# Optimization experiments

Measured on AMD Instinct MI355X. Metric: run time of the kernel, lower is better.

Reference implementation:

```python
import jax, jax.numpy as jnp
import numpy as np

BATCH = 8192
IN_F = 1024
OUT_F = 1024
GRID = 5
K = 3            # spline order (degree)
SCALE = 1.0      # scale_spline


def setup_inputs() -> dict:
    key = jax.random.key(0)
    k1, k2, k3 = jax.random.split(key, 3)
    x = jax.random.normal(k1, (BATCH, IN_F), dtype=jnp.float32)
    # kaiming_uniform_(a=sqrt(5)) on (out,in) -> U(-1/sqrt(in), 1/sqrt(in))
    bound = 1.0 / np.sqrt(IN_F)
    base_weight = jax.random.uniform(k2, (OUT_F, IN_F), jnp.float32, -bound, bound)
    # normal(mean=0, std=0.1), shape (out, in, grid_size + spline_order)
    spline_weight = 0.1 * jax.random.normal(k3, (OUT_F, IN_F, GRID + K), dtype=jnp.float32)
    # extended knot vector: uniform grid on [-1,1] with spacing h, padded by K knots each side
    h = 2.0 / GRID
    knots = jnp.arange(-K, GRID + K + 1, dtype=jnp.float32) * h - 1.0  # (GRID+2K+1,)
    grid = jnp.tile(knots[None, :], (IN_F, 1))                          # (in, GRID+2K+1)
    return {"x": x, "base_weight": base_weight, "spline_weight": spline_weight, "grid": grid}


def _b_splines(x, grid, k):
    # x: (B, in), grid: (in, G+2k+1) -> basis: (B, in, G+k)
    xe = x[..., None]  # (B, in, 1)
    basis = ((xe >= grid[:, :-1]) & (xe < grid[:, 1:])).astype(x.dtype)  # degree-0, (B,in,G+2k)
    for p in range(1, k + 1):  # Cox-de Boor recursion, degree p
        left = (xe - grid[:, :-(p + 1)]) / (grid[:, p:-1] - grid[:, :-(p + 1)]) * basis[..., :-1]
        right = (grid[:, (p + 1):] - xe) / (grid[:, (p + 1):] - grid[:, 1:-p]) * basis[..., 1:]
        basis = left + right
    return basis


def reference(x, base_weight, spline_weight, grid):
    base = x @ base_weight.T                                   # (B, out)
    basis = _b_splines(x, grid, K)                             # (B, in, G+K)
    spline = jnp.einsum('bic,oic->bo', basis, spline_weight)   # (B, out)
    return base + SCALE * spline
```

## Files before the change

kernel.cpp:

```cpp
#include <hip/hip_runtime.h>


#define BATCH 8192
#define IN_F  1024
#define OUT_F 1024
#define NC    9
#define KAUG  (IN_F * NC)

typedef float  f32x4  __attribute__((ext_vector_type(4)));
typedef __bf16 bf16x8 __attribute__((ext_vector_type(8)));
typedef unsigned short u16;
typedef u16 u16x8 __attribute__((ext_vector_type(8)));

__device__ __forceinline__ u16 f2bf(float f) {
  unsigned int u = __builtin_bit_cast(unsigned int, f);
  u += 0x7FFFu + ((u >> 16) & 1u);
  return (u16)(u >> 16);
}

#define KT(j) ((float)((j) - 3) * 0.4f - 1.0f)

__device__ __forceinline__ void bspline8(float x, float bas[11]) {
#pragma unroll
  for (int j = 0; j < 11; ++j)
    bas[j] = (x >= KT(j) && x < KT(j + 1)) ? 1.0f : 0.0f;
#pragma unroll
  for (int p = 1; p <= 3; ++p) {
#pragma unroll
    for (int j = 0; j < 11 - p; ++j) {
      bas[j] = (x - KT(j)) * (1.0f / (KT(j + p) - KT(j))) * bas[j]
             + (KT(j + p + 1) - x) * (1.0f / (KT(j + p + 1) - KT(j + 1))) * bas[j + 1];
    }
  }
}

__global__ __launch_bounds__(256) void build_AW(const float* __restrict__ X,
                                                const float* __restrict__ BW,
                                                const float* __restrict__ SW,
                                                u16* __restrict__ Aa,
                                                u16* __restrict__ Wa) {
  const int idx = blockIdx.x * 256 + threadIdx.x;
  if (idx < BATCH * 128) {
    const int b  = idx >> 7;
    const int i0 = (idx & 127) << 3;
    const float4* xp = (const float4*)(X + (size_t)b * IN_F + i0);
    float4 xa = xp[0], xb = xp[1];
    float xs[8] = {xa.x, xa.y, xa.z, xa.w, xb.x, xb.y, xb.z, xb.w};
    u16x8 out[9];
#pragma unroll
    for (int e = 0; e < 8; ++e) {
      const float x = xs[e];
      out[0][e] = f2bf(x);
      float bas[11];
      bspline8(x, bas);
#pragma unroll
      for (int c = 0; c < 8; ++c) out[c + 1][e] = f2bf(bas[c]);
    }
    u16* row = Aa + (size_t)b * KAUG + i0;
#pragma unroll
    for (int c = 0; c < 9; ++c) *(u16x8*)(row + c * IN_F) = out[c];
  } else {
    const int wdx = idx - BATCH * 128;
    const int o  = wdx >> 7;
    const int i0 = (wdx & 127) << 3;
    u16x8 out[9];
    const float4* bp = (const float4*)(BW + (size_t)o * IN_F + i0);
    float4 b0 = bp[0], b1 = bp[1];
    float bs[8] = {b0.x, b0.y, b0.z, b0.w, b1.x, b1.y, b1.z, b1.w};
#pragma unroll
    for (int e = 0; e < 8; ++e) out[0][e] = f2bf(bs[e]);
    const float4* sp = (const float4*)(SW + ((size_t)o * IN_F + i0) * 8);
#pragma unroll
    for (int e = 0; e < 8; ++e) {
      float4 s0 = sp[e * 2], s1 = sp[e * 2 + 1];
      out[1][e] = f2bf(s0.x);
      out[2][e] = f2bf(s0.y);
      out[3][e] = f2bf(s0.z);
      out[4][e] = f2bf(s0.w);
      out[5][e] = f2bf(s1.x);
      out[6][e] = f2bf(s1.y);
      out[7][e] = f2bf(s1.z);
      out[8][e] = f2bf(s1.w);
    }
    u16* row = Wa + (size_t)o * KAUG + i0;
#pragma unroll
    for (int c = 0; c < 9; ++c) *(u16x8*)(row + c * IN_F) = out[c];
  }
}

#define BM 256
#define BN 128
#define BK 64
#define NT (KAUG / BK)

__device__ __forceinline__ void async16(const u16* g, u16* l) {
  __builtin_amdgcn_global_load_lds(
      (const __attribute__((address_space(1))) u16*)g,
      (__attribute__((address_space(3))) u16*)l,
      16, 0, 0);
}

__global__ __launch_bounds__(512) void gemm_bt(
    const u16* __restrict__ A,
    const u16* __restrict__ B,
    float* __restrict__ C) {
  constexpr int N = OUT_F, K = KAUG;
  __shared__ __align__(16) u16 sm[3][24576];

  const int tid = threadIdx.x;

  const int bid = blockIdx.x;
  const int wg  = (bid & 7) * 32 + (bid >> 3);
  const int bm  = wg >> 3;
  const int bn  = wg & 7;

  const int lane = tid & 63;
  const int wid  = tid >> 6;
  const int wm   = wid >> 1;
  const int wn   = wid & 1;
  const int fr   = lane & 15;
  const int hi   = lane >> 4;

  const int ak0 = ((hi      ^ (fr & 7)) << 3);
  const int ak1 = (((4 | hi) ^ (fr & 7)) << 3);
  int arow[4], brow[4];
#pragma unroll
  for (int m = 0; m < 4; ++m) arow[m] = (wm * 64 + m * 16 + fr) * 64;
#pragma unroll
  for (int n = 0; n < 4; ++n) brow[n] = 16384 + (wn * 64 + n * 16 + fr) * 64;

  const int trow = tid >> 3;
  const int gsrc = (tid & 7) ^ (trow & 7);
  const u16* Asrc = A + (size_t)(bm * BM + trow) * K + gsrc * 8;
  const u16* Bsrc = B + (size_t)(bn * BN + trow) * K + gsrc * 8;

#pragma unroll
  for (int tt = 0; tt < 2; ++tt) {
    u16* dA = &sm[tt][0] + tid * 8;
    u16* dB = &sm[tt][16384] + tid * 8;
    const size_t kg = (size_t)tt * BK;
    async16(Asrc + kg, dA);
    async16(Asrc + (size_t)64  * K + kg, dA + 4096);
    async16(Asrc + (size_t)128 * K + kg, dA + 8192);
    async16(Asrc + (size_t)192 * K + kg, dA + 12288);
    async16(Bsrc + kg, dB);
    async16(Bsrc + (size_t)64  * K + kg, dB + 4096);
  }

  f32x4 acc[4][4] = {};

  for (int t = 0; t < NT; ++t) {
    const int cur = t % 3;
    const int nxt = (t + 2) % 3;
    const bool pf = (t + 2) < NT;
    const size_t kg = (size_t)(t + 2) * BK;
    const u16* s0 = &sm[cur][0];
    u16* dA = &sm[nxt][0] + tid * 8;
    u16* dB = &sm[nxt][16384] + tid * 8;

    if (t < NT - 1) asm volatile("s_waitcnt vmcnt(6)" ::: "memory");
    else            asm volatile("s_waitcnt vmcnt(0)" ::: "memory");
    __builtin_amdgcn_s_barrier();
    __builtin_amdgcn_sched_barrier(0);

    bf16x8 aa[4], bf[4];
#pragma unroll
    for (int n = 0; n < 4; ++n) bf[n] = *(const bf16x8*)(s0 + brow[n] + ak0);
#pragma unroll
    for (int m = 0; m < 4; ++m) aa[m] = *(const bf16x8*)(s0 + arow[m] + ak0);
    if (pf) {
      async16(Asrc + kg, dA);
      async16(Asrc + (size_t)64  * K + kg, dA + 4096);
      async16(Asrc + (size_t)128 * K + kg, dA + 8192);
    }
    __builtin_amdgcn_s_setprio(1);
#pragma unroll
    for (int m = 0; m < 4; ++m)
#pragma unroll
      for (int n = 0; n < 4; ++n)
        acc[m][n] = __builtin_amdgcn_mfma_f32_16x16x32_bf16(aa[m], bf[n], acc[m][n], 0, 0, 0);
    __builtin_amdgcn_s_setprio(0);
#pragma unroll
    for (int n = 0; n < 4; ++n) bf[n] = *(const bf16x8*)(s0 + brow[n] + ak1);
#pragma unroll
    for (int m = 0; m < 4; ++m) aa[m] = *(const bf16x8*)(s0 + arow[m] + ak1);
    if (pf) {
      async16(Asrc + (size_t)192 * K + kg, dA + 12288);
      async16(Bsrc + kg, dB);
      async16(Bsrc + (size_t)64  * K + kg, dB + 4096);
    }
    __builtin_amdgcn_s_setprio(1);
#pragma unroll
    for (int m = 0; m < 4; ++m)
#pragma unroll
      for (int n = 0; n < 4; ++n)
        acc[m][n] = __builtin_amdgcn_mfma_f32_16x16x32_bf16(aa[m], bf[n], acc[m][n], 0, 0, 0);
    __builtin_amdgcn_s_setprio(0);
  }

  const int r0 = bm * BM + wm * 64 + hi * 4;
  const int c0 = bn * BN + wn * 64 + fr;
#pragma unroll
  for (int i = 0; i < 4; ++i)
#pragma unroll
    for (int j = 0; j < 4; ++j) {
      float* cp = C + (size_t)(r0 + i * 16) * N + (c0 + j * 16);
#pragma unroll
      for (int r = 0; r < 4; ++r) cp[(size_t)r * N] = acc[i][j][r];
    }
}

extern "C" void kernel_launch(void* const* d_in, const int* in_sizes, int n_in,
                              void* d_out, int out_size, void* d_ws, size_t ws_size,
                              hipStream_t stream) {
  const float* x  = (const float*)d_in[0];
  const float* bw = (const float*)d_in[1];
  const float* sw = (const float*)d_in[2];
  float* out = (float*)d_out;

  u16* Aaug = (u16*)d_ws;
  u16* Waug = Aaug + (size_t)BATCH * KAUG;

  build_AW<<<dim3((BATCH + OUT_F) * 128 / 256), 256, 0, stream>>>(x, bw, sw, Aaug, Waug);
  gemm_bt<<<dim3(BATCH / BM * (OUT_F / BN)), 512, 0, stream>>>(Aaug, Waug, out);
}
```

Before: 271.2 us.

## Load A operands directly from global into registers, keep only B in LDS

The A tile no longer goes through shared memory. Each wave loads its own A fragments straight from global memory into registers, double-buffered across k-steps, while B stays in a three-stage LDS pipeline. This cuts LDS use from 144KB to 48KB so launch_bounds(512,2) can allow two blocks per CU, and it removes the LDS write/read traffic for A. In exchange, A global reads are per-lane 16-byte strided accesses that rows in other waves duplicate, vmcnt accounting becomes more delicate, and register pressure grows.

```diff
diff --git a/kernel.cpp b/kernel.cpp
--- a/kernel.cpp
+++ b/kernel.cpp
@@ -100,12 +100,12 @@
       16, 0, 0);
 }
 
-__global__ __launch_bounds__(512) void gemm_bt(
+__global__ __launch_bounds__(512, 2) void gemm_bt(
     const u16* __restrict__ A,
     const u16* __restrict__ B,
     float* __restrict__ C) {
   constexpr int N = OUT_F, K = KAUG;
-  __shared__ __align__(16) u16 sm[3][24576];
+  __shared__ __align__(16) u16 smB[3][8192];
 
   const int tid = threadIdx.x;
 
@@ -123,79 +123,79 @@
 
   const int ak0 = ((hi      ^ (fr & 7)) << 3);
   const int ak1 = (((4 | hi) ^ (fr & 7)) << 3);
-  int arow[4], brow[4];
-#pragma unroll
-  for (int m = 0; m < 4; ++m) arow[m] = (wm * 64 + m * 16 + fr) * 64;
-#pragma unroll
-  for (int n = 0; n < 4; ++n) brow[n] = 16384 + (wn * 64 + n * 16 + fr) * 64;
+  int brow[4];
+#pragma unroll
+  for (int n = 0; n < 4; ++n) brow[n] = (wn * 64 + n * 16 + fr) * 64;
 
   const int trow = tid >> 3;
   const int gsrc = (tid & 7) ^ (trow & 7);
-  const u16* Asrc = A + (size_t)(bm * BM + trow) * K + gsrc * 8;
   const u16* Bsrc = B + (size_t)(bn * BN + trow) * K + gsrc * 8;
 
+  const u16* Abase = A + (size_t)(bm * BM + wm * 64 + fr) * K + hi * 8;
+
+  bf16x8 aA[4][2], aB[4][2];
+#pragma unroll
+  for (int m = 0; m < 4; ++m)
+#pragma unroll
+    for (int kc = 0; kc < 2; ++kc)
+      aA[m][kc] = *(const bf16x8*)(Abase + (size_t)m * 16 * K + kc * 32);
 #pragma unroll
   for (int tt = 0; tt < 2; ++tt) {
-    u16* dA = &sm[tt][0] + tid * 8;
-    u16* dB = &sm[tt][16384] + tid * 8;
-    const size_t kg = (size_t)tt * BK;
-    async16(Asrc + kg, dA);
-    async16(Asrc + (size_t)64  * K + kg, dA + 4096);
-    async16(Asrc + (size_t)128 * K + kg, dA + 8192);
-    async16(Asrc + (size_t)192 * K + kg, dA + 12288);
-    async16(Bsrc + kg, dB);
-    async16(Bsrc + (size_t)64  * K + kg, dB + 4096);
+    u16* dB = &smB[tt][tid * 8];
+    async16(Bsrc + tt * BK, dB);
+    async16(Bsrc + (size_t)64 * K + tt * BK, dB + 4096);
   }
 
   f32x4 acc[4][4] = {};
 
-  for (int t = 0; t < NT; ++t) {
-    const int cur = t % 3;
-    const int nxt = (t + 2) % 3;
-    const bool pf = (t + 2) < NT;
-    const size_t kg = (size_t)(t + 2) * BK;
-    const u16* s0 = &sm[cur][0];
-    u16* dA = &sm[nxt][0] + tid * 8;
-    u16* dB = &sm[nxt][16384] + tid * 8;
-
-    if (t < NT - 1) asm volatile("s_waitcnt vmcnt(6)" ::: "memory");
-    else            asm volatile("s_waitcnt vmcnt(0)" ::: "memory");
+  auto tile = [&](int t, bf16x8 (&cur)[4][2], bf16x8 (&nxt)[4][2]) {
+    const int cb = t % 3;
+    const int nb = (t + 2) % 3;
+    const u16* sB = &smB[cb][0];
+    u16* dB = &smB[nb][tid * 8];
+
+    if (t == 0)           asm volatile("s_waitcnt vmcnt(0)"  ::: "memory");
+    else if (t == NT - 1) asm volatile("s_waitcnt vmcnt(8)"  ::: "memory");
+    else                  asm volatile("s_waitcnt vmcnt(10)" ::: "memory");
     __builtin_amdgcn_s_barrier();
     __builtin_amdgcn_sched_barrier(0);
 
-    bf16x8 aa[4], bf[4];
-#pragma unroll
-    for (int n = 0; n < 4; ++n) bf[n] = *(const bf16x8*)(s0 + brow[n] + ak0);
-#pragma unroll
-    for (int m = 0; m < 4; ++m) aa[m] = *(const bf16x8*)(s0 + arow[m] + ak0);
-    if (pf) {
-      async16(Asrc + kg, dA);
-      async16(Asrc + (size_t)64  * K + kg, dA + 4096);
-      async16(Asrc + (size_t)128 * K + kg, dA + 8192);
+    bf16x8 bf[4];
+#pragma unroll
+    for (int n = 0; n < 4; ++n) bf[n] = *(const bf16x8*)(sB + brow[n] + ak0);
+    if (t + 1 < NT) {
+#pragma unroll
+      for (int m = 0; m < 4; ++m)
+#pragma unroll
+        for (int kc = 0; kc < 2; ++kc)
+          nxt[m][kc] = *(const bf16x8*)(Abase + (size_t)m * 16 * K + kc * 32
+                                        + (size_t)(t + 1) * BK);
     }
     __builtin_amdgcn_s_setprio(1);
 #pragma unroll
     for (int m = 0; m < 4; ++m)
 #pragma unroll
       for (int n = 0; n < 4; ++n)
-        acc[m][n] = __builtin_amdgcn_mfma_f32_16x16x32_bf16(aa[m], bf[n], acc[m][n], 0, 0, 0);
+        acc[m][n] = __builtin_amdgcn_mfma_f32_16x16x32_bf16(cur[m][0], bf[n], acc[m][n], 0, 0, 0);
     __builtin_amdgcn_s_setprio(0);
 #pragma unroll
-    for (int n = 0; n < 4; ++n) bf[n] = *(const bf16x8*)(s0 + brow[n] + ak1);
-#pragma unroll
-    for (int m = 0; m < 4; ++m) aa[m] = *(const bf16x8*)(s0 + arow[m] + ak1);
-    if (pf) {
-      async16(Asrc + (size_t)192 * K + kg, dA + 12288);
-      async16(Bsrc + kg, dB);
-      async16(Bsrc + (size_t)64  * K + kg, dB + 4096);
+    for (int n = 0; n < 4; ++n) bf[n] = *(const bf16x8*)(sB + brow[n] + ak1);
+    if (t + 2 < NT) {
+      async16(Bsrc + (size_t)(t + 2) * BK, dB);
+      async16(Bsrc + (size_t)64 * K + (size_t)(t + 2) * BK, dB + 4096);
     }
     __builtin_amdgcn_s_setprio(1);
 #pragma unroll
     for (int m = 0; m < 4; ++m)
 #pragma unroll
       for (int n = 0; n < 4; ++n)
-        acc[m][n] = __builtin_amdgcn_mfma_f32_16x16x32_bf16(aa[m], bf[n], acc[m][n], 0, 0, 0);
+        acc[m][n] = __builtin_amdgcn_mfma_f32_16x16x32_bf16(cur[m][1], bf[n], acc[m][n], 0, 0, 0);
     __builtin_amdgcn_s_setprio(0);
+  };
+
+  for (int t = 0; t < NT; t += 2) {
+    tile(t,     aA, aB);
+    tile(t + 1, aB, aA);
   }
 
   const int r0 = bm * BM + wm * 64 + hi * 4;
```

Measured after the change: 463.6 us. 1.71x slower.
